# Kernel optimization log

Measured on AMD Instinct MI355X. Metric: run time of the kernel, lower is better.

Reference implementation:

```python
import jax, jax.numpy as jnp
import numpy as np
from math import sqrt

H = 16
D_MODEL = 1024
D_K = D_MODEL // H
B, S = 2, 2048


def setup_inputs() -> dict:
    key = jax.random.key(0)
    ks = jax.random.split(key, 12)
    scale = 1.0 / sqrt(D_MODEL)
    inp = {
        "query": jax.random.normal(ks[0], (B, S, D_MODEL), jnp.float32),
        "key": jax.random.normal(ks[1], (B, S, D_MODEL), jnp.float32),
        "value": jax.random.normal(ks[2], (B, S, D_MODEL), jnp.float32),
        # causal mask [B, S, S]; module unsqueezes head dim itself
        "mask": jnp.broadcast_to(jnp.tril(jnp.ones((S, S), jnp.int32)), (B, S, S)),
        "Wq": jax.random.normal(ks[3], (D_MODEL, D_MODEL), jnp.float32) * scale,
        "bq": jnp.zeros((D_MODEL,), jnp.float32),
        "Wk": jax.random.normal(ks[4], (D_MODEL, D_MODEL), jnp.float32) * scale,
        "bk": jnp.zeros((D_MODEL,), jnp.float32),
        "Wv": jax.random.normal(ks[5], (D_MODEL, D_MODEL), jnp.float32) * scale,
        "bv": jnp.zeros((D_MODEL,), jnp.float32),
        "Wo": jax.random.normal(ks[6], (D_MODEL, D_MODEL), jnp.float32) * scale,
        "bo": jnp.zeros((D_MODEL,), jnp.float32),
    }
    return inp


def reference(query, key, value, mask, Wq, bq, Wk, bk, Wv, bv, Wo, bo):
    nb = query.shape[0]

    def proj(x, W, b):
        # nn.Linear: x @ W.T + b, then split heads -> [B, H, S, D_K]
        y = jnp.einsum('bsd,ed->bse', x, W) + b
        return y.reshape(nb, -1, H, D_K).transpose(0, 2, 1, 3)

    q = proj(query, Wq, bq)
    k = proj(key, Wk, bk)
    v = proj(value, Wv, bv)

    scores = jnp.einsum('bhqd,bhkd->bhqk', q, k) / sqrt(D_K)  # [B,H,S,S]
    scores = jnp.where(mask[:, None, :, :] == 0, -jnp.inf, scores)
    probs = jax.nn.softmax(scores, axis=-1)  # dropout in eval mode (identity)
    ctx = jnp.einsum('bhqk,bhkd->bhqd', probs, v)
    ctx = ctx.transpose(0, 2, 1, 3).reshape(nb, -1, H * D_K)
    return jnp.einsum('bsd,ed->bse', ctx, Wo) + bo
```

## Files before the change

### kernel.cpp

```cpp
#include <hip/hip_runtime.h>
#include <hip/hip_bf16.h>
#include <stdint.h>


#define H_ 16
#define DM 1024
#define DK_ 64
#define BB 2
#define SS 2048
#define PSTR 72

typedef __bf16 bf16x8 __attribute__((ext_vector_type(8)));
typedef __bf16 bf16x2_t __attribute__((ext_vector_type(2)));
typedef float f32x4 __attribute__((ext_vector_type(4)));

#define GLOAD_LDS16(g, l)                                            \
  __builtin_amdgcn_global_load_lds(                                  \
      (__attribute__((address_space(1))) void*)(g),                  \
      (__attribute__((address_space(3))) void*)(l), 16, 0, 0)

__device__ __forceinline__ unsigned short f2bf_u(float f) {
  unsigned int u = __float_as_uint(f);
  u += 0x7fffu + ((u >> 16) & 1u);
  return (unsigned short)(u >> 16);
}

__device__ __forceinline__ unsigned int pack_bf16(float a, float b) {
#if __has_builtin(__builtin_amdgcn_cvt_pk_bf16_f32)
  bf16x2_t v = __builtin_amdgcn_cvt_pk_bf16_f32(a, b);
  unsigned int u;
  __builtin_memcpy(&u, &v, 4);
  return u;
#else
  return (unsigned int)f2bf_u(a) | ((unsigned int)f2bf_u(b) << 16);
#endif
}

__device__ __forceinline__ float fexp2(float x) {
#if __has_builtin(__builtin_amdgcn_exp2f)
  return __builtin_amdgcn_exp2f(x);
#else
  return exp2f(x);
#endif
}

struct Cvt {
  const float* s[7];
  unsigned short* d[7];
  int n[7];
};

__global__ __launch_bounds__(256) void convert_kernel(Cvt c) {
  const int y = blockIdx.y;
  const float* __restrict__ src = c.s[y];
  unsigned short* __restrict__ dst = c.d[y];
  const int nv = c.n[y] >> 2;
  for (int i = blockIdx.x * 256 + threadIdx.x; i < nv; i += 1024 * 256) {
    float4 v = *(const float4*)(src + (size_t)i * 4);
    ushort4 o;
    o.x = f2bf_u(v.x); o.y = f2bf_u(v.y); o.z = f2bf_u(v.z); o.w = f2bf_u(v.w);
    *(ushort4*)(dst + (size_t)i * 4) = o;
  }
}

template <int TN>
__device__ __forceinline__ void gemm_dbuf(
    const unsigned short* __restrict__ A, const unsigned short* __restrict__ W,
    unsigned short* As, unsigned short* Bs, int m0, int n0,
    f32x4 (*acc)[TN / 32]) {
  constexpr int FW = TN / 32;
  const int tid = threadIdx.x;
  const int wave = tid >> 6, lane = tid & 63;
  const int lm = lane & 15, quad = lane >> 4;
  const int wm = (wave >> 1) * 64, wn = (wave & 1) * (16 * FW);
  const int srow = lane >> 2;
  const int scol = (lane & 3) * 8;

#pragma unroll
  for (int i = 0; i < 4; ++i)
#pragma unroll
    for (int j = 0; j < FW; ++j) {
      f32x4 z = {0.f, 0.f, 0.f, 0.f};
      acc[i][j] = z;
    }

#pragma unroll
  for (int cc = 0; cc < 2; ++cc) {
    int c = wave * 2 + cc;
    GLOAD_LDS16(A + (size_t)(m0 + c * 16 + srow) * DM + scol,
                As + c * 512 + lane * 8);
  }
  if (TN == 128) {
#pragma unroll
    for (int cc = 0; cc < 2; ++cc) {
      int c = wave * 2 + cc;
      GLOAD_LDS16(W + (size_t)(n0 + c * 16 + srow) * DM + scol,
                  Bs + c * 512 + lane * 8);
    }
  } else {
    GLOAD_LDS16(W + (size_t)(n0 + wave * 16 + srow) * DM + scol,
                Bs + wave * 512 + lane * 8);
  }

  for (int kt = 0; kt < DM / 32; ++kt) {
    __syncthreads();
    const int cur = kt & 1;
    const unsigned short* Ac = As + cur * (128 * 32);
    const unsigned short* Bc = Bs + cur * (TN * 32);
    if (kt + 1 < DM / 32) {
      unsigned short* An = As + (cur ^ 1) * (128 * 32);
      unsigned short* Bn = Bs + (cur ^ 1) * (TN * 32);
      const int kcol = (kt + 1) * 32 + scol;
#pragma unroll
      for (int cc = 0; cc < 2; ++cc) {
        int c = wave * 2 + cc;
        GLOAD_LDS16(A + (size_t)(m0 + c * 16 + srow) * DM + kcol,
                    An + c * 512 + lane * 8);
      }
      if (TN == 128) {
#pragma unroll
        for (int cc = 0; cc < 2; ++cc) {
          int c = wave * 2 + cc;
          GLOAD_LDS16(W + (size_t)(n0 + c * 16 + srow) * DM + kcol,
                      Bn + c * 512 + lane * 8);
        }
      } else {
        GLOAD_LDS16(W + (size_t)(n0 + wave * 16 + srow) * DM + kcol,
                    Bn + wave * 512 + lane * 8);
      }
    }
    bf16x8 af[4], bfr[FW];
#pragma unroll
    for (int i = 0; i < 4; ++i)
      af[i] = *(const bf16x8*)(Ac + (wm + i * 16 + lm) * 32 + quad * 8);
#pragma unroll
    for (int j = 0; j < FW; ++j)
      bfr[j] = *(const bf16x8*)(Bc + (wn + j * 16 + lm) * 32 + quad * 8);
#pragma unroll
    for (int i = 0; i < 4; ++i)
#pragma unroll
      for (int j = 0; j < FW; ++j)
        acc[i][j] = __builtin_amdgcn_mfma_f32_16x16x32_bf16(af[i], bfr[j],
                                                            acc[i][j], 0, 0, 0);
  }
}

__global__ __launch_bounds__(512, 2) void qkv_gemm(
    const unsigned short* Qi, const unsigned short* Ki, const unsigned short* Vi,
    const unsigned short* Wq, const unsigned short* Wk, const unsigned short* Wv,
    const float* bq, const float* bk, const float* bv,
    unsigned short* Qf, unsigned short* Kf, unsigned short* Vf) {
  __shared__ unsigned short As[2 * 32 * 512];
  __shared__ unsigned short Bs[2 * 32 * 512];
  const int p = blockIdx.x;
  const int c = p & 7, idx = p >> 3;
  const int x = idx & 3, yy = (idx >> 2) & 1, z = idx >> 3;
  const int y = c * 2 + yy;
  const int m0 = y * 256, n0 = x * 256;
  const unsigned short* A = z == 0 ? Qi : (z == 1 ? Ki : Vi);
  const unsigned short* W = z == 0 ? Wq : (z == 1 ? Wk : Wv);
  const float* bias = z == 0 ? bq : (z == 1 ? bk : bv);
  const float scale = z == 0 ? 0.125f : 1.0f;

  const int tid = threadIdx.x;
  const int wave = tid >> 6, lane = tid & 63;
  const int lm = lane & 15, quad = lane >> 4;
  const int srow = lane >> 2, scol = (lane & 3) * 8;
  const int wr = wave >> 2, wc = wave & 3;

  f32x4 acc[8][4];
#pragma unroll
  for (int i = 0; i < 8; ++i)
#pragma unroll
    for (int j = 0; j < 4; ++j) {
      f32x4 zz = {0.f, 0.f, 0.f, 0.f};
      acc[i][j] = zz;
    }

#pragma unroll
  for (int cc = 0; cc < 4; ++cc) {
    int ch = wave * 4 + cc, rc = ch >> 1, kk = ch & 1;
    GLOAD_LDS16(A + (size_t)(m0 + rc * 16 + srow) * DM + kk * 32 + scol,
                As + ch * 512 + lane * 8);
    GLOAD_LDS16(W + (size_t)(n0 + rc * 16 + srow) * DM + kk * 32 + scol,
                Bs + ch * 512 + lane * 8);
  }

  for (int kt = 0; kt < DM / 64; ++kt) {
    __syncthreads();
    const int cur = kt & 1;
    const unsigned short* Ac = As + cur * (32 * 512);
    const unsigned short* Bc = Bs + cur * (32 * 512);
    if (kt + 1 < DM / 64) {
      unsigned short* An = As + (cur ^ 1) * (32 * 512);
      unsigned short* Bn = Bs + (cur ^ 1) * (32 * 512);
      const int k0 = (kt + 1) * 64;
#pragma unroll
      for (int cc = 0; cc < 4; ++cc) {
        int ch = wave * 4 + cc, rc = ch >> 1, kk = ch & 1;
        GLOAD_LDS16(A + (size_t)(m0 + rc * 16 + srow) * DM + k0 + kk * 32 + scol,
                    An + ch * 512 + lane * 8);
        GLOAD_LDS16(W + (size_t)(n0 + rc * 16 + srow) * DM + k0 + kk * 32 + scol,
                    Bn + ch * 512 + lane * 8);
      }
    }
#pragma unroll
    for (int kk = 0; kk < 2; ++kk) {
      bf16x8 af[8], bfr[4];
#pragma unroll
      for (int i = 0; i < 8; ++i)
        af[i] = *(const bf16x8*)(Ac + ((wr * 8 + i) * 2 + kk) * 512 +
                                 lm * 32 + quad * 8);
#pragma unroll
      for (int j = 0; j < 4; ++j)
        bfr[j] = *(const bf16x8*)(Bc + ((wc * 4 + j) * 2 + kk) * 512 +
                                  lm * 32 + quad * 8);
#pragma unroll
      for (int i = 0; i < 8; ++i)
#pragma unroll
        for (int j = 0; j < 4; ++j)
          acc[i][j] = __builtin_amdgcn_mfma_f32_16x16x32_bf16(
              af[i], bfr[j], acc[i][j], 0, 0, 0);
    }
  }

  if (z == 2) {
#pragma unroll
    for (int j = 0; j < 4; ++j) {
      int gn = n0 + wc * 64 + j * 16 + lm;
      float bv_ = bias[gn];
      int h2 = gn >> 6, dk = gn & 63;
      int a = dk >> 4, ln = dk & 15;
#pragma unroll
      for (int i = 0; i < 8; ++i) {
        int s0 = m0 + wr * 128 + i * 16 + quad * 4;
        int b2 = s0 >> 11, sl = s0 & 2047;
        int kt2 = sl >> 6, cc2 = (sl >> 5) & 1, qk = (sl >> 3) & 3, j0 = sl & 7;
        size_t base =
            ((size_t)(((b2 * 16 + h2) * 32 + kt2) * 4 + a) * 2 + cc2) * 512 +
            (qk * 16 + ln) * 8 + j0;
        uint2 w;
        w.x = pack_bf16(acc[i][j][0] + bv_, acc[i][j][1] + bv_);
        w.y = pack_bf16(acc[i][j][2] + bv_, acc[i][j][3] + bv_);
        *(uint2*)(Vf + base) = w;
      }
    }
  } else {
    unsigned short* out = z == 0 ? Qf : Kf;
#pragma unroll
    for (int j = 0; j < 4; ++j) {
      int gn = n0 + wc * 64 + j * 16 + lm;
      float bv_ = bias[gn];
      int h2 = gn >> 6, d64 = gn & 63;
      int cc2 = (d64 >> 5) & 1, qk = (d64 >> 3) & 3, jjq = d64 & 7;
#pragma unroll
      for (int i = 0; i < 8; ++i)
#pragma unroll
        for (int r = 0; r < 4; ++r) {
          int gm = m0 + wr * 128 + i * 16 + quad * 4 + r;
          int b2 = gm >> 11, sl = gm & 2047;
          size_t base =
              ((size_t)((b2 * 16 + h2) * 128 + (sl >> 4)) * 2 + cc2) * 512 +
              (qk * 16 + (sl & 15)) * 8 + jjq;
          out[base] = f2bf_u((acc[i][j][r] + bv_) * scale);
        }
    }
  }
}

__global__ __launch_bounds__(256) void o_gemm(
    const unsigned short* Ctx, const unsigned short* Wo, const float* bo,
    float* out) {
  __shared__ unsigned short As[2 * 128 * 32], Bs[2 * 64 * 32];
  const int p = blockIdx.x;
  const int c = p & 7, j0 = p >> 3;
  const int x = j0 & 15, yy = j0 >> 4;
  const int y = c * 4 + yy;
  const int m0 = y * 128, n0 = x * 64;
  f32x4 acc[4][2];
  gemm_dbuf<64>(Ctx, Wo, As, Bs, m0, n0, acc);
  const int lane = threadIdx.x & 63, wave = threadIdx.x >> 6;
  const int lm = lane & 15, quad = lane >> 4;
  const int wm = (wave >> 1) * 64, wn = (wave & 1) * 32;
#pragma unroll
  for (int j = 0; j < 2; ++j) {
    int gn = n0 + wn + j * 16 + lm;
    float bv_ = bo[gn];
#pragma unroll
    for (int i = 0; i < 4; ++i)
#pragma unroll
      for (int r = 0; r < 4; ++r) {
        int gm = m0 + wm + i * 16 + quad * 4 + r;
        out[(size_t)gm * DM + gn] = acc[i][j][r] + bv_;
      }
  }
}

__global__ __launch_bounds__(256, 4) void attn_kernel(
    const unsigned short* __restrict__ Qf, const unsigned short* __restrict__ Kf,
    const unsigned short* __restrict__ Vf, unsigned short* __restrict__ Ctx) {
  __shared__ unsigned short Ps[4][16 * PSTR];
  const int p = blockIdx.x;
  const int bh = p & 31, qb0 = p >> 5;
  const int qb = (bh & 1) ? (31 - qb0) : qb0;
  const int b = bh >> 4, h = bh & 15;
  const int tid = threadIdx.x, wave = tid >> 6, lane = tid & 63;
  const int lm = lane & 15, quad = lane >> 4;
  const float L2E = 1.4426950408889634f;

  const int qbase = qb * 64 + wave * 16;
  const int nkw = qb + 1;

  bf16x8 qf[2];
#pragma unroll
  for (int c = 0; c < 2; ++c)
    qf[c] = *(const bf16x8*)(Qf +
        ((size_t)(bh * 128 + (qbase >> 4)) * 2 + c) * 512 + lane * 8);

  const unsigned short* Kb = Kf + (size_t)bh * 256 * 512;
  const unsigned short* Vb = Vf + (size_t)bh * 256 * 512;
  unsigned short* Pw = Ps[wave];

  float lsum = 0.f;
  f32x4 oacc[4];
#pragma unroll
  for (int a = 0; a < 4; ++a) {
    f32x4 z = {0.f, 0.f, 0.f, 0.f};
    oacc[a] = z;
  }

  for (int kt = 0; kt < nkw; ++kt) {
    bf16x8 kf[4][2];
#pragma unroll
    for (int ik = 0; ik < 4; ++ik)
#pragma unroll
      for (int c = 0; c < 2; ++c)
        kf[ik][c] = *(const bf16x8*)(Kb +
            ((size_t)(kt * 4 + ik) * 2 + c) * 512 + lane * 8);
    f32x4 s[4];
#pragma unroll
    for (int ik = 0; ik < 4; ++ik) {
      f32x4 z = {0.f, 0.f, 0.f, 0.f};
      z = __builtin_amdgcn_mfma_f32_16x16x32_bf16(kf[ik][0], qf[0], z, 0, 0, 0);
      s[ik] = __builtin_amdgcn_mfma_f32_16x16x32_bf16(kf[ik][1], qf[1], z, 0, 0, 0);
    }
    if (kt == nkw - 1) {
#pragma unroll
      for (int ik = 0; ik < 4; ++ik)
#pragma unroll
        for (int r = 0; r < 4; ++r) {
          int kg = kt * 64 + ik * 16 + quad * 4 + r;
          int qg = qbase + lm;
          if (kg > qg) s[ik][r] = -1e30f;
        }
    }

    bf16x8 vf[4][2];
#pragma unroll
    for (int a = 0; a < 4; ++a)
#pragma unroll
      for (int c = 0; c < 2; ++c)
        vf[a][c] = *(const bf16x8*)(Vb +
            ((size_t)(kt * 8 + a * 2 + c)) * 512 + lane * 8);

#pragma unroll
    for (int ik = 0; ik < 4; ++ik) {
      float p0 = fexp2(s[ik][0] * L2E);
      float p1 = fexp2(s[ik][1] * L2E);
      float p2 = fexp2(s[ik][2] * L2E);
      float p3 = fexp2(s[ik][3] * L2E);
      lsum += (p0 + p1) + (p2 + p3);
      uint2 w;
      w.x = pack_bf16(p0, p1);
      w.y = pack_bf16(p2, p3);
      *(uint2*)(Pw + lm * PSTR + ik * 16 + quad * 4) = w;
    }

    bf16x8 pf[2];
#pragma unroll
    for (int c = 0; c < 2; ++c)
      pf[c] = *(const bf16x8*)(Pw + lm * PSTR + c * 32 + quad * 8);
#pragma unroll
    for (int a = 0; a < 4; ++a) {
      oacc[a] = __builtin_amdgcn_mfma_f32_16x16x32_bf16(pf[0], vf[a][0], oacc[a], 0, 0, 0);
      oacc[a] = __builtin_amdgcn_mfma_f32_16x16x32_bf16(pf[1], vf[a][1], oacc[a], 0, 0, 0);
    }
  }

  lsum += __shfl_xor(lsum, 16);
  lsum += __shfl_xor(lsum, 32);
#pragma unroll
  for (int r = 0; r < 4; ++r) {
    float inv = 1.0f / __shfl(lsum, quad * 4 + r);
    int qg = qbase + quad * 4 + r;
#pragma unroll
    for (int a = 0; a < 4; ++a)
      Ctx[(size_t)(b * SS + qg) * DM + h * DK_ + a * 16 + lm] =
          f2bf_u(oacc[a][r] * inv);
  }
}

extern "C" void kernel_launch(void* const* d_in, const int* in_sizes, int n_in,
                              void* d_out, int out_size, void* d_ws, size_t ws_size,
                              hipStream_t stream) {
  const float* q = (const float*)d_in[0];
  const float* k = (const float*)d_in[1];
  const float* v = (const float*)d_in[2];
  const float* Wq = (const float*)d_in[4];
  const float* bq = (const float*)d_in[5];
  const float* Wk = (const float*)d_in[6];
  const float* bk = (const float*)d_in[7];
  const float* Wv = (const float*)d_in[8];
  const float* bv = (const float*)d_in[9];
  const float* Wo = (const float*)d_in[10];
  const float* bo = (const float*)d_in[11];

  const size_t NX = (size_t)BB * SS * DM;
  const size_t NW = (size_t)DM * DM;
  unsigned short* ws = (unsigned short*)d_ws;
  unsigned short* Qi = ws;
  unsigned short* Ki = Qi + NX;
  unsigned short* Vi = Ki + NX;
  unsigned short* Wqb = Vi + NX;
  unsigned short* Wkb = Wqb + NW;
  unsigned short* Wvb = Wkb + NW;
  unsigned short* Wob = Wvb + NW;
  unsigned short* Qfr = Wob + NW;
  unsigned short* Kfr = Qfr + NX;
  unsigned short* Vfr = Kfr + NX;
  unsigned short* Ctx = Vfr + NX;

  Cvt c;
  c.s[0] = q; c.s[1] = k; c.s[2] = v; c.s[3] = Wq; c.s[4] = Wk; c.s[5] = Wv; c.s[6] = Wo;
  c.d[0] = Qi; c.d[1] = Ki; c.d[2] = Vi; c.d[3] = Wqb; c.d[4] = Wkb; c.d[5] = Wvb; c.d[6] = Wob;
  c.n[0] = c.n[1] = c.n[2] = (int)NX;
  c.n[3] = c.n[4] = c.n[5] = c.n[6] = (int)NW;

  convert_kernel<<<dim3(1024, 7), dim3(256), 0, stream>>>(c);
  qkv_gemm<<<dim3(192), dim3(512), 0, stream>>>(Qi, Ki, Vi, Wqb, Wkb, Wvb,
                                                bq, bk, bv, Qfr, Kfr, Vfr);
  attn_kernel<<<dim3(1024), dim3(256), 0, stream>>>(Qfr, Kfr, Vfr, Ctx);
  o_gemm<<<dim3(512), dim3(256), 0, stream>>>(Ctx, Wob, bo, (float*)d_out);
}
```

Measured before the change: 254.7 us.

## Restructure QKV GEMM mainloop with interleaved prefetch, swizzled LDS and MFMA priority

Rewrites the QKV projection GEMM main loop into a finely staged schedule. Half-K tile loads are issued between MFMA groups, with barriers, sched_barriers and explicit vmcnt waits so global-to-LDS traffic overlaps compute. An XOR swizzle on LDS column placement is added to reduce bank conflicts on the fragment reads, and s_setprio raises wave priority during MFMA bursts. The cost is a much more intricate hand-tuned schedule with extra barriers and a separate epilogue for the final two tiles; any mistake in the load/wait ordering would be a correctness hazard.

New measurement: 240.2 us. 1.06x faster.

```diff
diff --git a/kernel.cpp b/kernel.cpp
--- a/kernel.cpp
+++ b/kernel.cpp
@@ -150,8 +150,8 @@
     const unsigned short* Wq, const unsigned short* Wk, const unsigned short* Wv,
     const float* bq, const float* bk, const float* bv,
     unsigned short* Qf, unsigned short* Kf, unsigned short* Vf) {
-  __shared__ unsigned short As[2 * 32 * 512];
-  __shared__ unsigned short Bs[2 * 32 * 512];
+  __shared__ unsigned short As[2 * 2 * 16 * 512];
+  __shared__ unsigned short Bs[2 * 2 * 16 * 512];
   const int p = blockIdx.x;
   const int c = p & 7, idx = p >> 3;
   const int x = idx & 3, yy = (idx >> 2) & 1, z = idx >> 3;
@@ -165,8 +165,16 @@
   const int tid = threadIdx.x;
   const int wave = tid >> 6, lane = tid & 63;
   const int lm = lane & 15, quad = lane >> 4;
-  const int srow = lane >> 2, scol = (lane & 3) * 8;
   const int wr = wave >> 2, wc = wave & 3;
+
+  const int scs = 8 * ((lane & 3) ^ ((lane >> 3) & 3));
+  const size_t asrc0 = (size_t)(m0 + wave * 16 + (lane >> 2)) * DM + scs;
+  const size_t bsrc0 = (size_t)(n0 + wave * 16 + (lane >> 2)) * DM + scs;
+  const int sdst = wave * 512 + lane * 8;
+
+  const int rcol = (quad * 8) ^ (((lm >> 1) & 3) * 8);
+  const int aoff = wr * 8 * 512 + lm * 32 + rcol;
+  const int boff = wc * 4 * 512 + lm * 32 + rcol;
 
   f32x4 acc[8][4];
 #pragma unroll
@@ -177,52 +185,102 @@
       acc[i][j] = zz;
     }
 
-#pragma unroll
-  for (int cc = 0; cc < 4; ++cc) {
-    int ch = wave * 4 + cc, rc = ch >> 1, kk = ch & 1;
-    GLOAD_LDS16(A + (size_t)(m0 + rc * 16 + srow) * DM + kk * 32 + scol,
-                As + ch * 512 + lane * 8);
-    GLOAD_LDS16(W + (size_t)(n0 + rc * 16 + srow) * DM + kk * 32 + scol,
-                Bs + ch * 512 + lane * 8);
-  }
-
-  for (int kt = 0; kt < DM / 64; ++kt) {
-    __syncthreads();
-    const int cur = kt & 1;
-    const unsigned short* Ac = As + cur * (32 * 512);
-    const unsigned short* Bc = Bs + cur * (32 * 512);
-    if (kt + 1 < DM / 64) {
-      unsigned short* An = As + (cur ^ 1) * (32 * 512);
-      unsigned short* Bn = Bs + (cur ^ 1) * (32 * 512);
-      const int k0 = (kt + 1) * 64;
-#pragma unroll
-      for (int cc = 0; cc < 4; ++cc) {
-        int ch = wave * 4 + cc, rc = ch >> 1, kk = ch & 1;
-        GLOAD_LDS16(A + (size_t)(m0 + rc * 16 + srow) * DM + k0 + kk * 32 + scol,
-                    An + ch * 512 + lane * 8);
-        GLOAD_LDS16(W + (size_t)(n0 + rc * 16 + srow) * DM + k0 + kk * 32 + scol,
-                    Bn + ch * 512 + lane * 8);
-      }
-    }
-#pragma unroll
-    for (int kk = 0; kk < 2; ++kk) {
-      bf16x8 af[8], bfr[4];
+  auto stA = [&](int buf, int kh, int kt) {
+    const unsigned short* s = A + asrc0 + (size_t)kt * 64 + kh * 32;
+    unsigned short* d = As + buf * 16384 + kh * 8192 + sdst;
+    GLOAD_LDS16(s, d);
+    GLOAD_LDS16(s + (size_t)128 * DM, d + 4096);
+  };
+  auto stB = [&](int buf, int kh, int kt) {
+    const unsigned short* s = W + bsrc0 + (size_t)kt * 64 + kh * 32;
+    unsigned short* d = Bs + buf * 16384 + kh * 8192 + sdst;
+    GLOAD_LDS16(s, d);
+    GLOAD_LDS16(s + (size_t)128 * DM, d + 4096);
+  };
+
+  stA(0, 0, 0); stB(0, 0, 0); stA(0, 1, 0); stB(0, 1, 0);
+  stA(1, 0, 1); stB(1, 0, 1); stA(1, 1, 1);
+  asm volatile("s_waitcnt vmcnt(6)" ::: "memory");
+  __builtin_amdgcn_s_barrier();
+
+#define BARR __builtin_amdgcn_s_barrier()
+#define SCHB __builtin_amdgcn_sched_barrier(0)
+#define MFMA8(AF, B0_, B1_, J0, J1)                                          \
+  __builtin_amdgcn_s_setprio(1);                                             \
+  _Pragma("unroll")                                                          \
+  for (int i = 0; i < 8; ++i) {                                              \
+    acc[i][J0] = __builtin_amdgcn_mfma_f32_16x16x32_bf16(AF[i], B0_,         \
+                                                         acc[i][J0], 0, 0, 0); \
+    acc[i][J1] = __builtin_amdgcn_mfma_f32_16x16x32_bf16(AF[i], B1_,         \
+                                                         acc[i][J1], 0, 0, 0); \
+  }                                                                          \
+  __builtin_amdgcn_s_setprio(0)
+
+#pragma unroll 2
+  for (int t = 0; t < 14; ++t) {
+    const int buf = t & 1;
+    const unsigned short* Ab = As + buf * 16384;
+    const unsigned short* Bb = Bs + buf * 16384;
+    bf16x8 a0[8], b0[4];
+#pragma unroll
+    for (int i = 0; i < 8; ++i)
+      a0[i] = *(const bf16x8*)(Ab + aoff + i * 512);
+#pragma unroll
+    for (int j = 0; j < 4; ++j)
+      b0[j] = *(const bf16x8*)(Bb + boff + j * 512);
+    stB(buf ^ 1, 1, t + 1);
+    BARR; SCHB;
+    MFMA8(a0, b0[0], b0[1], 0, 1);
+    SCHB; BARR;
+    stA(buf, 0, t + 2);
+    BARR; SCHB;
+    MFMA8(a0, b0[2], b0[3], 2, 3);
+    SCHB; BARR;
+    bf16x8 a1[8], b1[4];
+#pragma unroll
+    for (int i = 0; i < 8; ++i)
+      a1[i] = *(const bf16x8*)(Ab + 8192 + aoff + i * 512);
+#pragma unroll
+    for (int j = 0; j < 4; ++j)
+      b1[j] = *(const bf16x8*)(Bb + 8192 + boff + j * 512);
+    stB(buf, 0, t + 2);
+    BARR; SCHB;
+    MFMA8(a1, b1[0], b1[1], 0, 1);
+    SCHB; BARR;
+    stA(buf, 1, t + 2);
+    asm volatile("s_waitcnt vmcnt(6)" ::: "memory");
+    BARR; SCHB;
+    MFMA8(a1, b1[2], b1[3], 2, 3);
+    SCHB; BARR;
+  }
+
+  stB(1, 1, 15);
+  asm volatile("s_waitcnt vmcnt(0)" ::: "memory");
+  __builtin_amdgcn_s_barrier();
+#pragma unroll
+  for (int tt = 0; tt < 2; ++tt) {
+    const unsigned short* Ab = As + tt * 16384;
+    const unsigned short* Bb = Bs + tt * 16384;
+#pragma unroll
+    for (int kh = 0; kh < 2; ++kh) {
+      bf16x8 a2[8], b2[4];
 #pragma unroll
       for (int i = 0; i < 8; ++i)
-        af[i] = *(const bf16x8*)(Ac + ((wr * 8 + i) * 2 + kk) * 512 +
-                                 lm * 32 + quad * 8);
+        a2[i] = *(const bf16x8*)(Ab + kh * 8192 + aoff + i * 512);
 #pragma unroll
       for (int j = 0; j < 4; ++j)
-        bfr[j] = *(const bf16x8*)(Bc + ((wc * 4 + j) * 2 + kk) * 512 +
-                                  lm * 32 + quad * 8);
+        b2[j] = *(const bf16x8*)(Bb + kh * 8192 + boff + j * 512);
 #pragma unroll
       for (int i = 0; i < 8; ++i)
 #pragma unroll
         for (int j = 0; j < 4; ++j)
           acc[i][j] = __builtin_amdgcn_mfma_f32_16x16x32_bf16(
-              af[i], bfr[j], acc[i][j], 0, 0, 0);
-    }
-  }
+              a2[i], b2[j], acc[i][j], 0, 0, 0);
+    }
+  }
+#undef MFMA8
+#undef SCHB
+#undef BARR
 
   if (z == 2) {
 #pragma unroll
```
